# Kernel optimization log

Measured on AMD Instinct MI355X. Metric: run time of the kernel, lower is better.

Reference implementation:

```python
import jax, jax.numpy as jnp
import numpy as np

H_SIZE = 1024
N_HEADS = 16
D_K = H_SIZE // N_HEADS


def setup_inputs() -> dict:
    key = jax.random.key(0)
    ks = jax.random.split(key, 12)
    s = 1.0 / np.sqrt(H_SIZE)
    inp = {
        "x": jax.random.normal(ks[0], (2, 2048, H_SIZE), dtype=jnp.float32),
        "Wq": jax.random.uniform(ks[1], (H_SIZE, H_SIZE), minval=-s, maxval=s),
        "bq": jax.random.uniform(ks[2], (H_SIZE,), minval=-s, maxval=s),
        "Wk": jax.random.uniform(ks[3], (H_SIZE, H_SIZE), minval=-s, maxval=s),
        "bk": jax.random.uniform(ks[4], (H_SIZE,), minval=-s, maxval=s),
        "Wv": jax.random.uniform(ks[5], (H_SIZE, H_SIZE), minval=-s, maxval=s),
        "bv": jax.random.uniform(ks[6], (H_SIZE,), minval=-s, maxval=s),
        "Wo": jax.random.uniform(ks[7], (H_SIZE, H_SIZE), minval=-s, maxval=s),
        "bo": jax.random.uniform(ks[8], (H_SIZE,), minval=-s, maxval=s),
        "ln_gamma": jnp.ones((H_SIZE,), dtype=jnp.float32),
        "ln_beta": jnp.zeros((H_SIZE,), dtype=jnp.float32),
    }
    return inp


def reference(x, Wq, bq, Wk, bk, Wv, bv, Wo, bo, ln_gamma, ln_beta):
    B, L, H = x.shape
    residual = x
    # QKV projections -> [B, n_heads, L, d_k]
    def proj(W, b):
        return (x @ W.T + b).reshape(B, L, N_HEADS, D_K).transpose(0, 2, 1, 3)
    q = proj(Wq, bq)
    k = proj(Wk, bk)
    v = proj(Wv, bv)
    # scaled dot-product attention (dropout = identity in eval mode)
    scores = jnp.einsum("bhqd,bhkd->bhqk", q, k) / jnp.sqrt(jnp.float32(D_K))
    attn = jax.nn.softmax(scores, axis=-1)
    out = jnp.einsum("bhqk,bhkd->bhqd", attn, v)
    out = out.transpose(0, 2, 1, 3).reshape(B, L, H)
    out = out @ Wo.T + bo
    # residual + LayerNorm
    y = out + residual
    mu = jnp.mean(y, axis=-1, keepdims=True)
    var = jnp.var(y, axis=-1, keepdims=True)
    y = (y - mu) / jnp.sqrt(var + 1e-5) * ln_gamma + ln_beta
    return y
```

## Files before the change

### kernel.cpp

```cpp
#include <hip/hip_runtime.h>

#define H_SIZE 1024
#define N_HEADS 16
#define D_K 64
#define SEQ 2048
#define BATCH 2
#define M_TOT 4096

typedef __bf16 __attribute__((ext_vector_type(8))) bf16_8;
typedef float __attribute__((ext_vector_type(4))) f32x4;
typedef float __attribute__((ext_vector_type(16))) f32x16;
typedef int __attribute__((ext_vector_type(4))) int4v;

#define SWZ(r) ((((r) & 7) ^ (((r) >> 3) & 7)))

__device__ __forceinline__ ushort f2bf(float f) {
    unsigned int u = __float_as_uint(f);
    unsigned int r = (u + 0x7FFFu + ((u >> 16) & 1u)) >> 16;
    return (ushort)r;
}

__device__ __forceinline__ unsigned int cvtpk(float lo, float hi) {
    unsigned int r;
    asm("v_cvt_pk_bf16_f32 %0, %1, %2" : "=v"(r) : "v"(lo), "v"(hi));
    return r;
}

__device__ __forceinline__ float exp2_raw(float x) {
    float r;
    asm("v_exp_f32 %0, %1" : "=v"(r) : "v"(x));
    return r;
}

__device__ __forceinline__ void gld16(void* lds, const void* g) {
    __builtin_amdgcn_global_load_lds(
        (const __attribute__((address_space(1))) unsigned int*)g,
        (__attribute__((address_space(3))) unsigned int*)lds, 16, 0, 0);
}

__global__ __launch_bounds__(256) void cast_all_kernel(
    const float* __restrict__ x, const float* __restrict__ wq, const float* __restrict__ wk,
    const float* __restrict__ wv, const float* __restrict__ wo,
    ushort* __restrict__ xb, ushort* __restrict__ wqb, ushort* __restrict__ wkb,
    ushort* __restrict__ wvb, ushort* __restrict__ wob) {
    int i = blockIdx.x * 256 + threadIdx.x;
    const float* src;
    ushort* dst;
    int off;
    if (i < 1048576) {
        src = x; dst = xb; off = i;
    } else {
        int j = i - 1048576;
        int w = j >> 18;
        off = j & 262143;
        src = (w == 0) ? wq : (w == 1) ? wk : (w == 2) ? wv : wo;
        dst = (w == 0) ? wqb : (w == 1) ? wkb : (w == 2) ? wvb : wob;
    }
    float4 v = ((const float4*)src)[off];
    ushort4 o;
    o.x = f2bf(v.x); o.y = f2bf(v.y); o.z = f2bf(v.z); o.w = f2bf(v.w);
    ((ushort4*)dst)[off] = o;
}

__global__ __launch_bounds__(256) void gemm_qkv(
    const ushort* __restrict__ A, const ushort* __restrict__ wq,
    const ushort* __restrict__ wk, const ushort* __restrict__ wv,
    const float* __restrict__ bq, const float* __restrict__ bk, const float* __restrict__ bv,
    ushort* __restrict__ Qb, ushort* __restrict__ Kb, ushort* __restrict__ Vtb) {
    constexpr int BK = 32;
    __shared__ ushort As[3][128 * BK];
    __shared__ ushort Bs[3][128 * BK];
    const int tid = threadIdx.x;
    const int lane = tid & 63, wid = tid >> 6;
    const int wr = wid >> 1, wc = wid & 1;
    const int hi = lane >> 4, lo = lane & 15;
    const int bm0 = blockIdx.x * 128;
    const int t3 = blockIdx.y >> 3;
    const int bn0 = (blockIdx.y & 7) * 128;
    const ushort* Bw = (t3 == 0) ? wq : (t3 == 1) ? wk : wv;
    const float* bias = (t3 == 0) ? bq : (t3 == 1) ? bk : bv;

    f32x4 acc[4][4] = {};

    const int srow = tid >> 2;
    const int sseg = ((tid & 3) ^ ((tid >> 3) & 3)) * 8;
    const ushort* gaB = A + (size_t)(bm0 + srow) * H_SIZE + sseg;
    const ushort* gbB = Bw + (size_t)(bn0 + srow) * H_SIZE + sseg;
    const int ldsOff = tid * 16;

#define STAGE(ba, bb, kt)                                 \
    {                                                     \
        char* la = (char*)(ba) + ldsOff;                  \
        char* lb = (char*)(bb) + ldsOff;                  \
        gld16(la, gaB + (kt));                            \
        gld16(la + 4096, gaB + 64 * H_SIZE + (kt));       \
        gld16(lb, gbB + (kt));                            \
        gld16(lb + 4096, gbB + 64 * H_SIZE + (kt));       \
    }

    STAGE(&As[0][0], &Bs[0][0], 0);
    STAGE(&As[1][0], &Bs[1][0], BK);
    asm volatile("s_waitcnt vmcnt(4)" ::: "memory");
    __builtin_amdgcn_s_barrier();
    __builtin_amdgcn_sched_barrier(0);

    constexpr int NT = H_SIZE / BK;
    const int rxv = (lo >> 1) & 3;
    int cur = 0;
    for (int t = 0; t < NT; t++) {
        int c2 = cur + 2; if (c2 >= 3) c2 -= 3;
        if (t + 2 < NT) STAGE(&As[c2][0], &Bs[c2][0], (t + 2) * BK);
        {
            bf16_8 af[4], bfv[4];
            const ushort* pa = &As[cur][(wr * 64 + lo) * BK + ((hi ^ rxv) * 8)];
            const ushort* pb = &Bs[cur][(wc * 64 + lo) * BK + ((hi ^ rxv) * 8)];
#pragma unroll
            for (int i = 0; i < 4; i++) af[i] = *(const bf16_8*)(pa + i * 16 * BK);
#pragma unroll
            for (int i = 0; i < 4; i++) bfv[i] = *(const bf16_8*)(pb + i * 16 * BK);
#pragma unroll
            for (int mi = 0; mi < 4; mi++)
#pragma unroll
                for (int ni = 0; ni < 4; ni++)
                    acc[mi][ni] = __builtin_amdgcn_mfma_f32_16x16x32_bf16(
                        af[mi], bfv[ni], acc[mi][ni], 0, 0, 0);
        }
        if (t + 1 < NT) {
            if (t + 2 < NT) { asm volatile("s_waitcnt vmcnt(4)" ::: "memory"); }
            else            { asm volatile("s_waitcnt vmcnt(0)" ::: "memory"); }
            __builtin_amdgcn_s_barrier();
            __builtin_amdgcn_sched_barrier(0);
        }
        cur = cur + 1; if (cur >= 3) cur -= 3;
    }
#undef STAGE

#pragma unroll
    for (int mi = 0; mi < 4; mi++) {
#pragma unroll
        for (int ni = 0; ni < 4; ni++) {
            const int row0 = bm0 + wr * 64 + mi * 16 + hi * 4;
            const int col = bn0 + wc * 64 + ni * 16 + lo;
            const float bv = bias[col];
            const int h = col >> 6, dk = col & 63;
            if (t3 == 2) {
                const int b = row0 >> 11, l0 = row0 & 2047;
                const int lsw0 = (l0 & ~63) | (((((l0 >> 3) & 7) ^ SWZ(dk)) & 7) << 3) | (l0 & 7);
                uint2 o;
                o.x = cvtpk(acc[mi][ni][0] + bv, acc[mi][ni][1] + bv);
                o.y = cvtpk(acc[mi][ni][2] + bv, acc[mi][ni][3] + bv);
                *(uint2*)&Vtb[((size_t)(b * N_HEADS + h) * D_K + dk) * SEQ + lsw0] = o;
            } else {
#pragma unroll
                for (int rr = 0; rr < 4; rr++) {
                    const int m = row0 + rr;
                    const int b = m >> 11, l = m & 2047;
                    float val = acc[mi][ni][rr] + bv;
                    if (t3 == 0) {
                        Qb[((size_t)(b * N_HEADS + h) * SEQ + l) * D_K + dk] =
                            f2bf(val * 0.18033688f);
                    } else {
                        int dks = ((((dk >> 3) ^ SWZ(l & 63)) & 7) << 3) | (dk & 7);
                        Kb[((size_t)(b * N_HEADS + h) * SEQ + l) * D_K + dks] = f2bf(val);
                    }
                }
            }
        }
    }
}

__global__ __launch_bounds__(256) void gemm_o(const ushort* __restrict__ A,
                                              const ushort* __restrict__ Bw,
                                              const float* __restrict__ bias,
                                              const float* __restrict__ resid,
                                              float* __restrict__ outp) {
    constexpr int BK = 32;
    __shared__ ushort As[3][128 * BK];
    __shared__ ushort Bs[3][64 * BK];
    const int tid = threadIdx.x;
    const int lane = tid & 63, wid = tid >> 6;
    const int wr = wid >> 1, wc = wid & 1;
    const int hi = lane >> 4, lo = lane & 15;
    const int bm0 = blockIdx.x * 128, bn0 = blockIdx.y * 64;

    f32x4 acc[4][2] = {};

    const int srow = tid >> 2;
    const int sseg = ((tid & 3) ^ ((tid >> 3) & 3)) * 8;
    const ushort* gaB = A + (size_t)(bm0 + srow) * H_SIZE + sseg;
    const ushort* gbB = Bw + (size_t)(bn0 + srow) * H_SIZE + sseg;
    const int ldsOff = tid * 16;

#define STAGE(ba, bb, kt)                                 \
    {                                                     \
        char* la = (char*)(ba) + ldsOff;                  \
        gld16(la, gaB + (kt));                            \
        gld16(la + 4096, gaB + 64 * H_SIZE + (kt));       \
        gld16((char*)(bb) + ldsOff, gbB + (kt));          \
    }

    STAGE(&As[0][0], &Bs[0][0], 0);
    STAGE(&As[1][0], &Bs[1][0], BK);
    asm volatile("s_waitcnt vmcnt(3)" ::: "memory");
    __builtin_amdgcn_s_barrier();
    __builtin_amdgcn_sched_barrier(0);

    constexpr int NT = H_SIZE / BK;
    const int rxv = (lo >> 1) & 3;
    int cur = 0;
    for (int t = 0; t < NT; t++) {
        int c2 = cur + 2; if (c2 >= 3) c2 -= 3;
        if (t + 2 < NT) STAGE(&As[c2][0], &Bs[c2][0], (t + 2) * BK);
        {
            bf16_8 af[4], bfv[2];
            const ushort* pa = &As[cur][(wr * 64 + lo) * BK + ((hi ^ rxv) * 8)];
            const ushort* pb = &Bs[cur][(wc * 32 + lo) * BK + ((hi ^ rxv) * 8)];
#pragma unroll
            for (int i = 0; i < 4; i++) af[i] = *(const bf16_8*)(pa + i * 16 * BK);
#pragma unroll
            for (int i = 0; i < 2; i++) bfv[i] = *(const bf16_8*)(pb + i * 16 * BK);
#pragma unroll
            for (int mi = 0; mi < 4; mi++)
#pragma unroll
                for (int ni = 0; ni < 2; ni++)
                    acc[mi][ni] = __builtin_amdgcn_mfma_f32_16x16x32_bf16(
                        af[mi], bfv[ni], acc[mi][ni], 0, 0, 0);
        }
        if (t + 1 < NT) {
            if (t + 2 < NT) { asm volatile("s_waitcnt vmcnt(3)" ::: "memory"); }
            else            { asm volatile("s_waitcnt vmcnt(0)" ::: "memory"); }
            __builtin_amdgcn_s_barrier();
            __builtin_amdgcn_sched_barrier(0);
        }
        cur = cur + 1; if (cur >= 3) cur -= 3;
    }
#undef STAGE

#pragma unroll
    for (int mi = 0; mi < 4; mi++) {
#pragma unroll
        for (int ni = 0; ni < 2; ni++) {
            const int row0 = bm0 + wr * 64 + mi * 16 + hi * 4;
            const int col = bn0 + wc * 32 + ni * 16 + lo;
            const float bv = bias[col];
#pragma unroll
            for (int rr = 0; rr < 4; rr++) {
                const int m = row0 + rr;
                outp[(size_t)m * H_SIZE + col] =
                    acc[mi][ni][rr] + bv + resid[(size_t)m * H_SIZE + col];
            }
        }
    }
}

__global__ __launch_bounds__(256) void attn_kernel(const ushort* __restrict__ Q,
                                                   const ushort* __restrict__ Ksw,
                                                   const ushort* __restrict__ Vsw,
                                                   ushort* __restrict__ Op0,
                                                   ushort* __restrict__ Op1,
                                                   float* __restrict__ Lpart) {
    __shared__ ushort Ks[3][64 * 64];
    __shared__ ushort Vs[3][64 * 64];
    const int lane = threadIdx.x & 63, wid = threadIdx.x >> 6;
    const int h32 = lane >> 5, q32 = lane & 31;
    const int bh = blockIdx.y;
    const int z = blockIdx.z;
    const int q0w = blockIdx.x * 256 + wid * 64;
    const int kbase = z * (SEQ / 2);
    const ushort* Qh = Q + (size_t)bh * SEQ * D_K;
    const ushort* Kp = Ksw + (size_t)bh * SEQ * D_K;
    const ushort* Vp = Vsw + (size_t)bh * D_K * SEQ;

    bf16_8 qfA[4], qfB[4];
#pragma unroll
    for (int tt = 0; tt < 4; tt++) {
        qfA[tt] = *(const bf16_8*)(Qh + (size_t)(q0w + q32) * D_K + tt * 16 + h32 * 8);
        qfB[tt] = *(const bf16_8*)(Qh + (size_t)(q0w + 32 + q32) * D_K + tt * 16 + h32 * 8);
    }

    f32x16 oA0 = {}, oA1 = {}, oB0 = {}, oB1 = {};
    float lsA = 0.f, lsB = 0.f;

    const int koff = wid * 2048 + lane * 16;
    const int vrow = wid * 16 + (lane >> 3);
    const int vseg = (lane & 7) * 16;

#define STAGE(bb, kt)                                                             \
    {                                                                             \
        const char* kg = (const char*)(Kp + (size_t)(kt) * D_K);                  \
        char* kl = (char*)&Ks[bb][0];                                             \
        gld16(kl + koff, kg + koff);                                              \
        gld16(kl + koff + 1024, kg + koff + 1024);                                \
        char* vl = (char*)&Vs[bb][0];                                             \
        gld16(vl + vrow * 128 + vseg,                                             \
              (const char*)(Vp + (size_t)vrow * SEQ + (kt)) + vseg);              \
        gld16(vl + (vrow + 8) * 128 + vseg,                                       \
              (const char*)(Vp + (size_t)(vrow + 8) * SEQ + (kt)) + vseg);        \
    }

    STAGE(0, kbase);
    STAGE(1, kbase + 64);
    asm volatile("s_waitcnt vmcnt(4)" ::: "memory");
    __builtin_amdgcn_s_barrier();
    __builtin_amdgcn_sched_barrier(0);

    constexpr int NTT = (SEQ / 2) / 64;
    int cur = 0;
    for (int t = 0; t < NTT; t++) {
        int c2 = cur + 2; if (c2 >= 3) c2 -= 3;
        if (t + 2 < NTT) STAGE(c2, kbase + (t + 2) * 64);
        const ushort* kb = &Ks[cur][0];
        const ushort* vb = &Vs[cur][0];
#pragma unroll
        for (int kh = 0; kh < 2; kh++) {
            f32x16 stA = {}, stB = {};
            const int krow = kh * 32 + q32;
            __builtin_amdgcn_s_setprio(1);
#pragma unroll
            for (int tt = 0; tt < 4; tt++) {
                int sg = (2 * tt + h32) ^ SWZ(krow);
                bf16_8 kf = *(const bf16_8*)(kb + krow * 64 + sg * 8);
                stA = __builtin_amdgcn_mfma_f32_32x32x16_bf16(kf, qfA[tt], stA, 0, 0, 0);
                stB = __builtin_amdgcn_mfma_f32_32x32x16_bf16(kf, qfB[tt], stB, 0, 0, 0);
            }
            __builtin_amdgcn_s_setprio(0);

            union { unsigned int w[4]; bf16_8 v; } pfA0, pfA1, pfB0, pfB1;
            float partA = 0.f, partB = 0.f;
#pragma unroll
            for (int i = 0; i < 2; i++) {
                float a0 = exp2_raw(stA[2 * i]),     a1 = exp2_raw(stA[2 * i + 1]);
                float a2 = exp2_raw(stA[4 + 2 * i]), a3 = exp2_raw(stA[4 + 2 * i + 1]);
                partA += (a0 + a1) + (a2 + a3);
                unsigned int ua = cvtpk(a0, a1), ub = cvtpk(a2, a3);
                asm volatile("v_permlane32_swap_b32 %0, %1" : "+v"(ua), "+v"(ub));
                pfA0.w[i] = ua; pfA0.w[2 + i] = ub;
                float a4 = exp2_raw(stA[8 + 2 * i]),  a5 = exp2_raw(stA[8 + 2 * i + 1]);
                float a6 = exp2_raw(stA[12 + 2 * i]), a7 = exp2_raw(stA[12 + 2 * i + 1]);
                partA += (a4 + a5) + (a6 + a7);
                unsigned int uc = cvtpk(a4, a5), ud = cvtpk(a6, a7);
                asm volatile("v_permlane32_swap_b32 %0, %1" : "+v"(uc), "+v"(ud));
                pfA1.w[i] = uc; pfA1.w[2 + i] = ud;
                float b0 = exp2_raw(stB[2 * i]),     b1 = exp2_raw(stB[2 * i + 1]);
                float b2 = exp2_raw(stB[4 + 2 * i]), b3 = exp2_raw(stB[4 + 2 * i + 1]);
                partB += (b0 + b1) + (b2 + b3);
                unsigned int ue = cvtpk(b0, b1), uf = cvtpk(b2, b3);
                asm volatile("v_permlane32_swap_b32 %0, %1" : "+v"(ue), "+v"(uf));
                pfB0.w[i] = ue; pfB0.w[2 + i] = uf;
                float b4 = exp2_raw(stB[8 + 2 * i]),  b5 = exp2_raw(stB[8 + 2 * i + 1]);
                float b6 = exp2_raw(stB[12 + 2 * i]), b7 = exp2_raw(stB[12 + 2 * i + 1]);
                partB += (b4 + b5) + (b6 + b7);
                unsigned int ug = cvtpk(b4, b5), uh = cvtpk(b6, b7);
                asm volatile("v_permlane32_swap_b32 %0, %1" : "+v"(ug), "+v"(uh));
                pfB1.w[i] = ug; pfB1.w[2 + i] = uh;
            }
            lsA += partA + __shfl_xor(partA, 32);
            lsB += partB + __shfl_xor(partB, 32);

            __builtin_amdgcn_s_setprio(1);
            {
                const int vr0 = q32;
                int sg0 = (4 * kh + h32) ^ SWZ(vr0);
                int sg1 = (4 * kh + 2 + h32) ^ SWZ(vr0);
                bf16_8 vf0 = *(const bf16_8*)(vb + vr0 * 64 + sg0 * 8);
                bf16_8 vf1 = *(const bf16_8*)(vb + vr0 * 64 + sg1 * 8);
                oA0 = __builtin_amdgcn_mfma_f32_32x32x16_bf16(pfA0.v, vf0, oA0, 0, 0, 0);
                oB0 = __builtin_amdgcn_mfma_f32_32x32x16_bf16(pfB0.v, vf0, oB0, 0, 0, 0);
                oA0 = __builtin_amdgcn_mfma_f32_32x32x16_bf16(pfA1.v, vf1, oA0, 0, 0, 0);
                oB0 = __builtin_amdgcn_mfma_f32_32x32x16_bf16(pfB1.v, vf1, oB0, 0, 0, 0);
            }
            {
                const int vr1 = 32 + q32;
                int sg0 = (4 * kh + h32) ^ SWZ(vr1);
                int sg1 = (4 * kh + 2 + h32) ^ SWZ(vr1);
                bf16_8 vf0 = *(const bf16_8*)(vb + vr1 * 64 + sg0 * 8);
                bf16_8 vf1 = *(const bf16_8*)(vb + vr1 * 64 + sg1 * 8);
                oA1 = __builtin_amdgcn_mfma_f32_32x32x16_bf16(pfA0.v, vf0, oA1, 0, 0, 0);
                oB1 = __builtin_amdgcn_mfma_f32_32x32x16_bf16(pfB0.v, vf0, oB1, 0, 0, 0);
                oA1 = __builtin_amdgcn_mfma_f32_32x32x16_bf16(pfA1.v, vf1, oA1, 0, 0, 0);
                oB1 = __builtin_amdgcn_mfma_f32_32x32x16_bf16(pfB1.v, vf1, oB1, 0, 0, 0);
            }
            __builtin_amdgcn_s_setprio(0);
        }
        if (t + 1 < NTT) {
            if (t + 2 < NTT) { asm volatile("s_waitcnt vmcnt(4)" ::: "memory"); }
            else             { asm volatile("s_waitcnt vmcnt(0)" ::: "memory"); }
            __builtin_amdgcn_s_barrier();
            __builtin_amdgcn_sched_barrier(0);
        }
        cur = cur + 1; if (cur >= 3) cur -= 3;
    }
#undef STAGE

    ushort* Op = (z == 0) ? Op0 : Op1;
    float* Lp = Lpart + (size_t)z * N_HEADS * BATCH * SEQ;
    const int b = bh >> 4, h = bh & 15;
#pragma unroll
    for (int rr = 0; rr < 16; rr++) {
        const int qloc = (rr & 3) + 8 * (rr >> 2) + 4 * h32;
        const int lA = q0w + qloc;
        ushort* orowA = Op + ((size_t)(b * SEQ + lA)) * H_SIZE + h * 64;
        orowA[q32] = f2bf(oA0[rr]);
        orowA[32 + q32] = f2bf(oA1[rr]);
        const int lB = q0w + 32 + qloc;
        ushort* orowB = Op + ((size_t)(b * SEQ + lB)) * H_SIZE + h * 64;
        orowB[q32] = f2bf(oB0[rr]);
        orowB[32 + q32] = f2bf(oB1[rr]);
    }
    if (lane < 32) {
        Lp[(size_t)bh * SEQ + q0w + q32] = lsA;
        Lp[(size_t)bh * SEQ + q0w + 32 + q32] = lsB;
    }
}

__global__ __launch_bounds__(256) void combine_kernel(const ushort* __restrict__ O0,
                                                      const ushort* __restrict__ O1,
                                                      const float* __restrict__ Lp,
                                                      ushort* __restrict__ Ao) {
    int idx = blockIdx.x * 256 + threadIdx.x;
    int m = idx >> 7;
    int col0 = (idx & 127) * 8;
    int b = m >> 11, l = m & 2047, h = col0 >> 6;
    int bh = b * N_HEADS + h;
    float inv = 1.0f / (Lp[(size_t)bh * SEQ + l] +
                        Lp[(size_t)(N_HEADS * BATCH + bh) * SEQ + l]);
    size_t off = (size_t)m * H_SIZE + col0;
    int4v a = *(const int4v*)(O0 + off);
    int4v c = *(const int4v*)(O1 + off);
    unsigned int r[4];
#pragma unroll
    for (int j = 0; j < 4; j++) {
        unsigned int ua = (unsigned int)a[j], uc = (unsigned int)c[j];
        float lo = __uint_as_float(ua << 16) + __uint_as_float(uc << 16);
        float hi = __uint_as_float(ua & 0xFFFF0000u) + __uint_as_float(uc & 0xFFFF0000u);
        r[j] = cvtpk(lo * inv, hi * inv);
    }
    *(int4v*)(Ao + off) = *(const int4v*)r;
}

__global__ __launch_bounds__(256) void ln_kernel(float* __restrict__ y,
                                                 const float* __restrict__ gamma,
                                                 const float* __restrict__ beta) {
    const int row = blockIdx.x;
    float4* p = (float4*)(y + (size_t)row * H_SIZE);
    float4 v = p[threadIdx.x];
    float s = v.x + v.y + v.z + v.w;
    float s2 = v.x * v.x + v.y * v.y + v.z * v.z + v.w * v.w;
#pragma unroll
    for (int off = 1; off < 64; off <<= 1) {
        s += __shfl_xor(s, off);
        s2 += __shfl_xor(s2, off);
    }
    __shared__ float ss[4], ss2[4];
    const int wid = threadIdx.x >> 6, lane = threadIdx.x & 63;
    if (lane == 0) { ss[wid] = s; ss2[wid] = s2; }
    __syncthreads();
    s = ss[0] + ss[1] + ss[2] + ss[3];
    s2 = ss2[0] + ss2[1] + ss2[2] + ss2[3];
    const float mean = s * (1.0f / H_SIZE);
    const float var = s2 * (1.0f / H_SIZE) - mean * mean;
    const float rstd = rsqrtf(var + 1e-5f);
    const float4 g = ((const float4*)gamma)[threadIdx.x];
    const float4 bt = ((const float4*)beta)[threadIdx.x];
    float4 o;
    o.x = (v.x - mean) * rstd * g.x + bt.x;
    o.y = (v.y - mean) * rstd * g.y + bt.y;
    o.z = (v.z - mean) * rstd * g.z + bt.z;
    o.w = (v.w - mean) * rstd * g.w + bt.w;
    p[threadIdx.x] = o;
}

extern "C" void kernel_launch(void* const* d_in, const int* in_sizes, int n_in,
                              void* d_out, int out_size, void* d_ws, size_t ws_size,
                              hipStream_t stream) {
    const float* x = (const float*)d_in[0];
    const float* Wq = (const float*)d_in[1];
    const float* bq = (const float*)d_in[2];
    const float* Wk = (const float*)d_in[3];
    const float* bk = (const float*)d_in[4];
    const float* Wv = (const float*)d_in[5];
    const float* bv = (const float*)d_in[6];
    const float* Wo = (const float*)d_in[7];
    const float* bo = (const float*)d_in[8];
    const float* gamma = (const float*)d_in[9];
    const float* beta = (const float*)d_in[10];

    char* ws = (char*)d_ws;
    ushort* xb  = (ushort*)(ws);
    ushort* wqb = (ushort*)(ws + (8u << 20));
    ushort* wkb = (ushort*)(ws + (10u << 20));
    ushort* wvb = (ushort*)(ws + (12u << 20));
    ushort* wob = (ushort*)(ws + (14u << 20));
    ushort* Qb  = (ushort*)(ws + (16u << 20));
    ushort* Kb  = (ushort*)(ws + (24u << 20));
    ushort* Vtb = (ushort*)(ws + (32u << 20));
    ushort* Ao  = (ushort*)(ws + (40u << 20));
    ushort* Op0 = (ushort*)(ws);
    ushort* Op1 = Ao;
    float*  Lpt = (float*)(ws + (48u << 20));

    cast_all_kernel<<<8192, 256, 0, stream>>>(x, Wq, Wk, Wv, Wo, xb, wqb, wkb, wvb, wob);

    dim3 gq(M_TOT / 128, 24);
    gemm_qkv<<<gq, 256, 0, stream>>>(xb, wqb, wkb, wvb, bq, bk, bv, Qb, Kb, Vtb);

    dim3 g2(SEQ / 256, BATCH * N_HEADS, 2);
    attn_kernel<<<g2, 256, 0, stream>>>(Qb, Kb, Vtb, Op0, Op1, Lpt);

    combine_kernel<<<(M_TOT * H_SIZE / 8) / 256, 256, 0, stream>>>(Op0, Op1, Lpt, Ao);

    dim3 go(M_TOT / 128, H_SIZE / 64);
    gemm_o<<<go, 256, 0, stream>>>(Ao, wob, bo, x, (float*)d_out);

    ln_kernel<<<M_TOT, 256, 0, stream>>>((float*)d_out, gamma, beta);
}
```

Baseline: 137.9 us.

## Fuse split-KV attention combine into output projection GEMM A-tile load

Removes the separate combine kernel: gemm_o now loads the two partial attention outputs and the softmax denominators directly, normalizes and packs to bf16 in registers, and writes the A tile to LDS. The pipeline drops from triple-buffered async LDS loads to double buffering with a full vmcnt(0) wait each iteration. Each output-projection block recomputes the combine for its row tile, so the partials are re-read across all 16 column blocks. The attention kernel also remaps block indices so consecutive blocks are spread across heads, presumably for cache or scheduling locality.

```diff
diff --git a/kernel.cpp b/kernel.cpp
--- a/kernel.cpp
+++ b/kernel.cpp
@@ -169,14 +169,16 @@
     }
 }
 
-__global__ __launch_bounds__(256) void gemm_o(const ushort* __restrict__ A,
+__global__ __launch_bounds__(256) void gemm_o(const ushort* __restrict__ Op0,
+                                              const ushort* __restrict__ Op1,
+                                              const float* __restrict__ Lp,
                                               const ushort* __restrict__ Bw,
                                               const float* __restrict__ bias,
                                               const float* __restrict__ resid,
                                               float* __restrict__ outp) {
     constexpr int BK = 32;
-    __shared__ ushort As[3][128 * BK];
-    __shared__ ushort Bs[3][64 * BK];
+    __shared__ ushort As[2][128 * BK];
+    __shared__ ushort Bs[2][64 * BK];
     const int tid = threadIdx.x;
     const int lane = tid & 63, wid = tid >> 6;
     const int wr = wid >> 1, wc = wid & 1;
@@ -186,31 +188,66 @@
     f32x4 acc[4][2] = {};
 
     const int srow = tid >> 2;
-    const int sseg = ((tid & 3) ^ ((tid >> 3) & 3)) * 8;
-    const ushort* gaB = A + (size_t)(bm0 + srow) * H_SIZE + sseg;
-    const ushort* gbB = Bw + (size_t)(bn0 + srow) * H_SIZE + sseg;
-    const int ldsOff = tid * 16;
-
-#define STAGE(ba, bb, kt)                                 \
-    {                                                     \
-        char* la = (char*)(ba) + ldsOff;                  \
-        gld16(la, gaB + (kt));                            \
-        gld16(la + 4096, gaB + 64 * H_SIZE + (kt));       \
-        gld16((char*)(bb) + ldsOff, gbB + (kt));          \
-    }
-
-    STAGE(&As[0][0], &Bs[0][0], 0);
-    STAGE(&As[1][0], &Bs[1][0], BK);
-    asm volatile("s_waitcnt vmcnt(3)" ::: "memory");
-    __builtin_amdgcn_s_barrier();
-    __builtin_amdgcn_sched_barrier(0);
+    const int c4 = tid & 3;
+    const int pseg = (c4 ^ ((srow >> 1) & 3)) * 8;
+    const int m0 = bm0 + srow, m1 = bm0 + srow + 64;
+    const int b0 = m0 >> 11, l0r = m0 & 2047;
+    const int b1 = m1 >> 11, l1r = m1 & 2047;
+    const ushort* gbB = Bw + (size_t)(bn0 + srow) * H_SIZE + pseg;
+
+    uint4 a0, a1, a2, a3;
+    float lp00, lp01, lp10, lp11;
+
+#define LOAD_AB(t1)                                                               \
+    {                                                                             \
+        gld16((char*)&Bs[(t1) & 1][0] + tid * 16, gbB + (t1) * BK);               \
+        const int colb = (t1) * BK + c4 * 8;                                      \
+        a0 = *(const uint4*)(Op0 + (size_t)m0 * H_SIZE + colb);                   \
+        a1 = *(const uint4*)(Op1 + (size_t)m0 * H_SIZE + colb);                   \
+        a2 = *(const uint4*)(Op0 + (size_t)m1 * H_SIZE + colb);                   \
+        a3 = *(const uint4*)(Op1 + (size_t)m1 * H_SIZE + colb);                   \
+        const int h = (t1) >> 1;                                                  \
+        lp00 = Lp[(size_t)(b0 * N_HEADS + h) * SEQ + l0r];                        \
+        lp01 = Lp[65536 + (size_t)(b0 * N_HEADS + h) * SEQ + l0r];                \
+        lp10 = Lp[(size_t)(b1 * N_HEADS + h) * SEQ + l1r];                        \
+        lp11 = Lp[65536 + (size_t)(b1 * N_HEADS + h) * SEQ + l1r];                \
+    }
+
+#define COMBINE_WRITE(t1)                                                         \
+    {                                                                             \
+        const float inv0 = 1.0f / (lp00 + lp01);                                  \
+        const float inv1 = 1.0f / (lp10 + lp11);                                  \
+        unsigned int w0[4], w1[4];                                                \
+        const unsigned int* pa = (const unsigned int*)&a0;                        \
+        const unsigned int* pc = (const unsigned int*)&a1;                        \
+        const unsigned int* pd = (const unsigned int*)&a2;                        \
+        const unsigned int* pe = (const unsigned int*)&a3;                        \
+        _Pragma("unroll")                                                         \
+        for (int j = 0; j < 4; j++) {                                             \
+            float vlo = __uint_as_float(pa[j] << 16) + __uint_as_float(pc[j] << 16); \
+            float vhi = __uint_as_float(pa[j] & 0xFFFF0000u) +                    \
+                        __uint_as_float(pc[j] & 0xFFFF0000u);                     \
+            w0[j] = cvtpk(vlo * inv0, vhi * inv0);                                \
+            float ulo = __uint_as_float(pd[j] << 16) + __uint_as_float(pe[j] << 16); \
+            float uhi = __uint_as_float(pd[j] & 0xFFFF0000u) +                    \
+                        __uint_as_float(pe[j] & 0xFFFF0000u);                     \
+            w1[j] = cvtpk(ulo * inv1, uhi * inv1);                                \
+        }                                                                         \
+        ushort* dst = &As[(t1) & 1][srow * BK + pseg];                            \
+        *(uint4*)dst = *(const uint4*)w0;                                         \
+        *(uint4*)(dst + 64 * BK) = *(const uint4*)w1;                             \
+    }
+
+    LOAD_AB(0);
+    asm volatile("s_waitcnt vmcnt(0)" ::: "memory");
+    COMBINE_WRITE(0);
+    __syncthreads();
 
     constexpr int NT = H_SIZE / BK;
     const int rxv = (lo >> 1) & 3;
-    int cur = 0;
     for (int t = 0; t < NT; t++) {
-        int c2 = cur + 2; if (c2 >= 3) c2 -= 3;
-        if (t + 2 < NT) STAGE(&As[c2][0], &Bs[c2][0], (t + 2) * BK);
+        const int cur = t & 1;
+        if (t + 1 < NT) LOAD_AB(t + 1);
         {
             bf16_8 af[4], bfv[2];
             const ushort* pa = &As[cur][(wr * 64 + lo) * BK + ((hi ^ rxv) * 8)];
@@ -227,14 +264,13 @@
                         af[mi], bfv[ni], acc[mi][ni], 0, 0, 0);
         }
         if (t + 1 < NT) {
-            if (t + 2 < NT) { asm volatile("s_waitcnt vmcnt(3)" ::: "memory"); }
-            else            { asm volatile("s_waitcnt vmcnt(0)" ::: "memory"); }
-            __builtin_amdgcn_s_barrier();
-            __builtin_amdgcn_sched_barrier(0);
-        }
-        cur = cur + 1; if (cur >= 3) cur -= 3;
-    }
-#undef STAGE
+            asm volatile("s_waitcnt vmcnt(0)" ::: "memory");
+            COMBINE_WRITE(t + 1);
+            __syncthreads();
+        }
+    }
+#undef LOAD_AB
+#undef COMBINE_WRITE
 
 #pragma unroll
     for (int mi = 0; mi < 4; mi++) {
@@ -263,9 +299,13 @@
     __shared__ ushort Vs[3][64 * 64];
     const int lane = threadIdx.x & 63, wid = threadIdx.x >> 6;
     const int h32 = lane >> 5, q32 = lane & 31;
-    const int bh = blockIdx.y;
+
+    const int lin = blockIdx.y * gridDim.x + blockIdx.x;
+    const int nlin = (lin & 7) * 32 + (lin >> 3);
+    const int bx = nlin & 7;
+    const int bh = nlin >> 3;
     const int z = blockIdx.z;
-    const int q0w = blockIdx.x * 256 + wid * 64;
+    const int q0w = bx * 256 + wid * 64;
     const int kbase = z * (SEQ / 2);
     const ushort* Qh = Q + (size_t)bh * SEQ * D_K;
     const ushort* Kp = Ksw + (size_t)bh * SEQ * D_K;
@@ -413,31 +453,6 @@
     }
 }
 
-__global__ __launch_bounds__(256) void combine_kernel(const ushort* __restrict__ O0,
-                                                      const ushort* __restrict__ O1,
-                                                      const float* __restrict__ Lp,
-                                                      ushort* __restrict__ Ao) {
-    int idx = blockIdx.x * 256 + threadIdx.x;
-    int m = idx >> 7;
-    int col0 = (idx & 127) * 8;
-    int b = m >> 11, l = m & 2047, h = col0 >> 6;
-    int bh = b * N_HEADS + h;
-    float inv = 1.0f / (Lp[(size_t)bh * SEQ + l] +
-                        Lp[(size_t)(N_HEADS * BATCH + bh) * SEQ + l]);
-    size_t off = (size_t)m * H_SIZE + col0;
-    int4v a = *(const int4v*)(O0 + off);
-    int4v c = *(const int4v*)(O1 + off);
-    unsigned int r[4];
-#pragma unroll
-    for (int j = 0; j < 4; j++) {
-        unsigned int ua = (unsigned int)a[j], uc = (unsigned int)c[j];
-        float lo = __uint_as_float(ua << 16) + __uint_as_float(uc << 16);
-        float hi = __uint_as_float(ua & 0xFFFF0000u) + __uint_as_float(uc & 0xFFFF0000u);
-        r[j] = cvtpk(lo * inv, hi * inv);
-    }
-    *(int4v*)(Ao + off) = *(const int4v*)r;
-}
-
 __global__ __launch_bounds__(256) void ln_kernel(float* __restrict__ y,
                                                  const float* __restrict__ gamma,
                                                  const float* __restrict__ beta) {
@@ -494,9 +509,8 @@
     ushort* Qb  = (ushort*)(ws + (16u << 20));
     ushort* Kb  = (ushort*)(ws + (24u << 20));
     ushort* Vtb = (ushort*)(ws + (32u << 20));
-    ushort* Ao  = (ushort*)(ws + (40u << 20));
     ushort* Op0 = (ushort*)(ws);
-    ushort* Op1 = Ao;
+    ushort* Op1 = (ushort*)(ws + (40u << 20));
     float*  Lpt = (float*)(ws + (48u << 20));
 
     cast_all_kernel<<<8192, 256, 0, stream>>>(x, Wq, Wk, Wv, Wo, xb, wqb, wkb, wvb, wob);
@@ -507,10 +521,8 @@
     dim3 g2(SEQ / 256, BATCH * N_HEADS, 2);
     attn_kernel<<<g2, 256, 0, stream>>>(Qb, Kb, Vtb, Op0, Op1, Lpt);
 
-    combine_kernel<<<(M_TOT * H_SIZE / 8) / 256, 256, 0, stream>>>(Op0, Op1, Lpt, Ao);
-
     dim3 go(M_TOT / 128, H_SIZE / 64);
-    gemm_o<<<go, 256, 0, stream>>>(Ao, wob, bo, x, (float*)d_out);
+    gemm_o<<<go, 256, 0, stream>>>(Op0, Op1, Lpt, wob, bo, x, (float*)d_out);
 
     ln_kernel<<<M_TOT, 256, 0, stream>>>((float*)d_out, gamma, beta);
 }
```

Result: slower. 152.4 us (+10.5%).
